# Kernel tuning notes

Hardware: AMD Instinct MI355X
Metric: run time of the kernel (lower is better)

Reference implementation:

```python
import jax, jax.numpy as jnp
import numpy as np

NOISE_EPS = 1e-2   # Shazeer noisy-gating stddev floor
LN_EPS = 1e-6
LOSS_COEF = 0.01
K = 2              # num_activated_experts


def _layer_norm(x, w, b):
    mu = jnp.mean(x, axis=-1, keepdims=True)
    var = jnp.var(x, axis=-1, keepdims=True)
    return (x - mu) * jax.lax.rsqrt(var + LN_EPS) * w + b


def _cv_squared(v):
    return jnp.var(v) / (jnp.mean(v) ** 2 + 1e-10)


def _normal_cdf(z):
    return 0.5 * (1.0 + jax.scipy.special.erf(z / jnp.sqrt(jnp.asarray(2.0, z.dtype))))


def setup_inputs() -> dict:
    key = jax.random.key(0)
    ks = jax.random.split(key, 8)
    N, D, H, O, E = 8192, 512, 1024, 512, 8
    x = jax.random.normal(ks[0], (N, D), jnp.float32)
    x_offsets = jnp.sort(jax.random.randint(ks[1], (17,), 0, N)).astype(jnp.int64)
    noise = jax.random.normal(ks[2], (N, E), jnp.float32)
    s = 0.02
    return {
        "x": x,
        "x_offsets": x_offsets,
        "max_seq_len": 2048,
        "noise": noise,
        "norm_w": jnp.ones((D,), jnp.float32),
        "norm_bias": jnp.zeros((D,), jnp.float32),
        "w_gate": jax.random.normal(ks[3], (D, E), jnp.float32) * s,
        "w_noise": jax.random.normal(ks[4], (D, E), jnp.float32) * s,
        "W1": jax.random.normal(ks[5], (E, H, D), jnp.float32) * s,  # [E, model_d, input]
        "b1": jnp.zeros((E, H), jnp.float32),
        "W2": jax.random.normal(ks[6], (E, O, H), jnp.float32) * s,  # [E, output, model_d]
        "b2": jnp.zeros((E, O), jnp.float32),
        "output_weight": jax.random.normal(ks[7], (D, O), jnp.float32) * s,
    }


def reference(x, x_offsets, max_seq_len, noise, norm_w, norm_bias, w_gate, w_noise,
              W1, b1, W2, b2, output_weight):
    N, D = x.shape
    E = w_gate.shape[1]
    k_plus = min(K + 1, E)

    # pre-norm
    x_norm = _layer_norm(x, norm_w, norm_bias)

    # noisy top-k gating (training path)
    clean_logits = x_norm @ w_gate                      # [N, E]
    noise_stddev = jax.nn.softplus(x_norm @ w_noise) + NOISE_EPS
    noisy_logits = clean_logits + noise * noise_stddev

    top_logits, top_indices = jax.lax.top_k(noisy_logits, k_plus)   # [N, k+1]
    top_k_logits = top_logits[:, :K]
    top_k_indices = top_indices[:, :K]
    top_k_gates = jax.nn.softmax(top_k_logits, axis=-1)             # [N, K]

    rows = jnp.arange(N)[:, None]
    gates = jnp.zeros((N, E), top_k_gates.dtype).at[rows, top_k_indices].set(top_k_gates)

    # load = prob each expert is in top-k under the gating noise (Shazeer)
    flat = top_logits.reshape(-1)
    pos_in = jnp.arange(N) * k_plus + K
    thr_in = flat[pos_in][:, None]          # (k+1)-th value: threshold if already in
    thr_out = flat[pos_in - 1][:, None]     # k-th value: threshold if currently out
    is_in = noisy_logits > thr_in
    prob_in = _normal_cdf((clean_logits - thr_in) / noise_stddev)
    prob_out = _normal_cdf((clean_logits - thr_out) / noise_stddev)
    load_probs = jnp.where(is_in, prob_in, prob_out)                # [N, E]

    loss = LOSS_COEF * (_cv_squared(gates.sum(0)) + _cv_squared(load_probs.sum(0)))

    # dispatch stats: tokens per expert
    lengths = jnp.zeros((E,), jnp.float32).at[top_k_indices.reshape(-1)].add(1.0)
    load = lengths / lengths.sum()

    # grouped expert MLP (dense one-hot combine; gates are 0 for unrouted experts)
    h = jnp.einsum('nd,ehd->neh', x_norm, W1) + b1                  # [N, E, H]
    a = jax.nn.silu(h)
    y_e = jnp.einsum('neh,eoh->neo', a, W2) + b2                    # [N, E, O]
    y_moe = jnp.einsum('ne,neo->no', gates, y_e)                    # [N, O]

    # shared expert: addmm(y, shared_x=x, output_weight)
    y = y_moe + x @ output_weight
    return y, loss, load
```

## Files before the change

### kernel.cpp

```cpp
#include <hip/hip_runtime.h>
#include <math.h>

typedef unsigned short u16;
typedef unsigned int u32;

#define N_ROWS 8192
#define DDIM 512
#define HDIM 1024
#define ODIM 512
#define NEXP 8
#define MAXPAIRS (N_ROWS * 2)
#define MAXPOS (MAXPAIRS + NEXP * 128)
#define MAXTILES (MAXPOS / 128)

#define SM_CNT 0
#define SM_CUR 8
#define SM_AOFF 16
#define SM_GSUM 32
#define SM_LSUM 40
#define SM_WORDS 64

using short8 = __attribute__((ext_vector_type(8))) short;
using float4v = __attribute__((ext_vector_type(4))) float;

__device__ __forceinline__ u16 f2bf(float f) {
    union { float f; u32 u; } v; v.f = f;
    u32 u = v.u;
    return (u16)((u + 0x7fffu + ((u >> 16) & 1u)) >> 16);
}

__device__ __forceinline__ void async_copy16(u16* lds, const u16* g) {
    __builtin_amdgcn_global_load_lds(
        (const __attribute__((address_space(1))) void*)g,
        (__attribute__((address_space(3))) void*)lds, 16, 0, 0);
}

#define CONV_BLOCKS 8192
__global__ __launch_bounds__(256) void prep_kernel(
    const float* __restrict__ W1, const float* __restrict__ W2, const float* __restrict__ ow,
    u16* __restrict__ W1b, u16* __restrict__ W2b, u16* __restrict__ owT,
    int* __restrict__ small, int* __restrict__ bucket_rows, float* __restrict__ zeropage)
{
    __shared__ float tile[32][33];
    int b = blockIdx.x, tid = threadIdx.x;
    if (b < CONV_BLOCKS) {
        const size_t n4 = (size_t)NEXP * HDIM * DDIM / 4;
        size_t i = (size_t)b * 256 + tid;
        const float* src; u16* dst;
        if (i < n4) { src = W1; dst = W1b; } else { src = W2; dst = W2b; i -= n4; }
        float4 v = ((const float4*)src)[i];
        ushort4 o;
        o.x = f2bf(v.x); o.y = f2bf(v.y); o.z = f2bf(v.z); o.w = f2bf(v.w);
        ((ushort4*)dst)[i] = o;
    } else if (b < CONV_BLOCKS + 256) {
        int t = b - CONV_BLOCKS;
        int bx = (t & 15) * 32, by = (t >> 4) * 32;
        int tx = tid & 31, ty = tid >> 5;
        for (int r = ty; r < 32; r += 8) tile[r][tx] = ow[(size_t)(by + r) * ODIM + bx + tx];
        __syncthreads();
        for (int r = ty; r < 32; r += 8) owT[(size_t)(bx + r) * DDIM + by + tx] = f2bf(tile[tx][r]);
    } else {
        int i = (b - CONV_BLOCKS - 256) * 256 + tid;
        if (i < SM_WORDS) small[i] = 0;
        if (i < 512) zeropage[i] = 0.f;
        if (i < MAXPOS) bucket_rows[i] = -1;
    }
}

__global__ __launch_bounds__(256) void gating_kernel(
    const float* __restrict__ x, const float* __restrict__ noise,
    const float* __restrict__ norm_w, const float* __restrict__ norm_b,
    const float* __restrict__ w_gate, const float* __restrict__ w_noise,
    u16* __restrict__ xnorm_bf, u16* __restrict__ x_bf,
    int* __restrict__ pair_expert, float* __restrict__ pair_gate,
    int* __restrict__ small)
{
    __shared__ float wgT[NEXP * DDIM];
    __shared__ float wnT[NEXP * DDIM];
    __shared__ float blk_g[NEXP];
    __shared__ float blk_l[NEXP];
    __shared__ int blk_c[NEXP];
    float* smf = (float*)small;

    int tid = threadIdx.x;
    for (int i = tid; i < NEXP * DDIM; i += 256) {
        int d = i >> 3, e = i & 7;
        wgT[e * DDIM + d] = w_gate[i];
        wnT[e * DDIM + d] = w_noise[i];
    }
    if (tid < NEXP) { blk_g[tid] = 0.f; blk_l[tid] = 0.f; blk_c[tid] = 0; }
    __syncthreads();

    int wave = tid >> 6, lane = tid & 63;
    float nw[8], nb[8];
#pragma unroll
    for (int j = 0; j < 8; j++) { nw[j] = norm_w[j * 64 + lane]; nb[j] = norm_b[j * 64 + lane]; }

    for (int r = 0; r < 4; ++r) {
        int row = blockIdx.x * 16 + wave * 4 + r;
        const float* xr = x + (size_t)row * DDIM;
        float xv[8], s = 0.f, s2 = 0.f;
#pragma unroll
        for (int j = 0; j < 8; j++) { float v = xr[j * 64 + lane]; xv[j] = v; s += v; s2 += v * v; }
#pragma unroll
        for (int o = 32; o; o >>= 1) { s += __shfl_xor(s, o, 64); s2 += __shfl_xor(s2, o, 64); }
        float mu = s * (1.f / DDIM);
        float var = s2 * (1.f / DDIM) - mu * mu;
        float rstd = rsqrtf(var + 1e-6f);

        float acc[16];
#pragma unroll
        for (int e = 0; e < 16; e++) acc[e] = 0.f;
#pragma unroll
        for (int j = 0; j < 8; j++) {
            float v = (xv[j] - mu) * rstd * nw[j] + nb[j];
            int d = j * 64 + lane;
            xnorm_bf[(size_t)row * DDIM + d] = f2bf(v);
            x_bf[(size_t)row * DDIM + d] = f2bf(xv[j]);
#pragma unroll
            for (int e = 0; e < 8; e++) {
                acc[e] += v * wgT[e * DDIM + d];
                acc[8 + e] += v * wnT[e * DDIM + d];
            }
        }
#pragma unroll
        for (int e = 0; e < 16; e++)
#pragma unroll
            for (int o = 32; o; o >>= 1) acc[e] += __shfl_xor(acc[e], o, 64);

        float cl[8], sd[8], nz[8];
#pragma unroll
        for (int e = 0; e < 8; e++) {
            cl[e] = acc[e];
            float t = acc[8 + e];
            float sp = fmaxf(t, 0.f) + log1pf(expf(-fabsf(t)));
            sd[e] = sp + 0.01f;
            nz[e] = cl[e] + noise[(size_t)row * NEXP + e] * sd[e];
        }
        int idx[3]; float val[3]; u32 msk = 0;
#pragma unroll
        for (int t = 0; t < 3; t++) {
            float best = -INFINITY; int bi = 0;
#pragma unroll
            for (int e = 0; e < 8; e++)
                if (!((msk >> e) & 1) && nz[e] > best) { best = nz[e]; bi = e; }
            idx[t] = bi; val[t] = best; msk |= 1u << bi;
        }
        float e1 = expf(val[1] - val[0]);
        float g0 = 1.f / (1.f + e1), g1 = e1 / (1.f + e1);
        float thr_in = val[2], thr_out = val[1];

        if (lane == 0) {
            pair_expert[row * 2] = idx[0]; pair_gate[row * 2] = g0;
            pair_expert[row * 2 + 1] = idx[1]; pair_gate[row * 2 + 1] = g1;
            atomicAdd(&blk_g[idx[0]], g0); atomicAdd(&blk_g[idx[1]], g1);
            atomicAdd(&blk_c[idx[0]], 1); atomicAdd(&blk_c[idx[1]], 1);
#pragma unroll
            for (int e = 0; e < 8; e++) {
                float thr = (nz[e] > thr_in) ? thr_in : thr_out;
                float z = (cl[e] - thr) / sd[e];
                float p = 0.5f * (1.f + erff(z * 0.70710678118654752f));
                atomicAdd(&blk_l[e], p);
            }
        }
    }
    __syncthreads();
    if (tid < NEXP) {
        atomicAdd(smf + SM_GSUM + tid, blk_g[tid]);
        atomicAdd(smf + SM_LSUM + tid, blk_l[tid]);
        atomicAdd(&small[SM_CNT + tid], blk_c[tid]);
    }
}

__global__ __launch_bounds__(256) void scatter_kernel(
    const int* __restrict__ pair_expert, const float* __restrict__ pair_gate,
    int* __restrict__ small, int* __restrict__ bucket_rows, float* __restrict__ gate_by_pos,
    float* __restrict__ out_loss, float* __restrict__ out_load)
{
    __shared__ int aoff[NEXP + 1];
    __shared__ int blk_cnt[NEXP];
    __shared__ int blk_base[NEXP];
    int tid = threadIdx.x;
    if (tid == 0) {
        int acc = 0; aoff[0] = 0;
        for (int e = 0; e < NEXP; e++) { acc += (small[SM_CNT + e] + 127) & ~127; aoff[e + 1] = acc; }
    }
    if (tid < NEXP) blk_cnt[tid] = 0;
    __syncthreads();
    int p = blockIdx.x * 256 + tid;
    int e = pair_expert[p];
    int local = atomicAdd(&blk_cnt[e], 1);
    __syncthreads();
    if (tid < NEXP)
        blk_base[tid] = aoff[tid] + atomicAdd(&small[SM_CUR + tid], blk_cnt[tid]);
    if (blockIdx.x == 0 && tid < NEXP + 1) small[SM_AOFF + tid] = aoff[tid];
    __syncthreads();
    int pos = blk_base[e] + local;
    bucket_rows[pos] = p >> 1;
    gate_by_pos[pos] = pair_gate[p];

    if (blockIdx.x == 0 && tid == 0) {
        const float* gs = (const float*)small + SM_GSUM;
        const float* ls = (const float*)small + SM_LSUM;
        float cv[2];
        for (int t = 0; t < 2; t++) {
            const float* v = t ? ls : gs;
            float m = 0.f;
            for (int k = 0; k < NEXP; k++) m += v[k];
            m *= (1.f / NEXP);
            float var = 0.f;
            for (int k = 0; k < NEXP; k++) { float d = v[k] - m; var += d * d; }
            var *= (1.f / NEXP);
            cv[t] = var / (m * m + 1e-10f);
        }
        out_loss[0] = 0.01f * (cv[0] + cv[1]);
        int tot = 0;
        for (int k = 0; k < NEXP; k++) tot += small[SM_CNT + k];
        float inv = 1.f / (float)tot;
        for (int k = 0; k < NEXP; k++) out_load[k] = (float)small[SM_CNT + k] * inv;
    }
}



__global__ __launch_bounds__(256) void gemmA_kernel(
    const u16* __restrict__ xnorm, const u16* __restrict__ xbf,
    const u16* __restrict__ W1b, const u16* __restrict__ owT,
    const int* __restrict__ bucket_rows, const int* __restrict__ small,
    const float* __restrict__ b1, const u16* __restrict__ zeropage,
    u16* __restrict__ a_buf, float* __restrict__ y)
{
    constexpr int KD = 512;
    __shared__ __align__(16) u16 As[128 * 64];
    __shared__ __align__(16) u16 Bs[128 * 64];

    int tid = threadIdx.x;
    bool m0 = blockIdx.y < 8;
    int base, bn, e = 0;
    const u16* Bsel;
    if (m0) {
        base = blockIdx.x * 128;
        if (base >= small[SM_AOFF + 8]) return;
        while (e < 7 && base >= small[SM_AOFF + e + 1]) ++e;
        bn = blockIdx.y * 128;
        Bsel = W1b + (size_t)e * HDIM * KD;
    } else {
        int j = (blockIdx.y - 8) * 136 + blockIdx.x;
        if (j >= 256) return;
        base = (j >> 2) * 128;
        bn = (j & 3) * 128;
        Bsel = owT;
    }

    int wave = tid >> 6, lane = tid & 63;
    int lr = lane >> 3;
    int lc = ((lane & 7) ^ lr) * 8;

    const u16* ga[4]; const u16* gb[4];
    u16* la[4]; u16* lb[4];
#pragma unroll
    for (int c = 0; c < 4; c++) {
        int tr = wave * 32 + c * 8;
        if (m0) {
            int r0 = bucket_rows[base + tr + lr];
            ga[c] = ((r0 < 0) ? zeropage : xnorm + (size_t)r0 * KD) + lc;
        } else {
            ga[c] = xbf + (size_t)(base + tr + lr) * KD + lc;
        }
        gb[c] = Bsel + (size_t)(bn + tr + lr) * KD + lc;
        la[c] = &As[tr * 64];
        lb[c] = &Bs[tr * 64];
    }

    int wm = (wave & 1) * 64, wn = (wave >> 1) * 64;
    int fr = lane & 15, kq = lane >> 4, f7 = fr & 7;

    float4v acc[4][4];
#pragma unroll
    for (int i = 0; i < 4; i++)
#pragma unroll
        for (int j = 0; j < 4; j++) acc[i][j] = (float4v){0.f, 0.f, 0.f, 0.f};

    for (int k0 = 0; k0 < KD; k0 += 64) {
        __syncthreads();
#pragma unroll
        for (int c = 0; c < 4; c++) async_copy16(la[c], ga[c] + k0);
#pragma unroll
        for (int c = 0; c < 4; c++) async_copy16(lb[c], gb[c] + k0);
        __syncthreads();
        short8 af[4][2], bf[4][2];
#pragma unroll
        for (int mt = 0; mt < 4; mt++)
#pragma unroll
            for (int kh = 0; kh < 2; kh++)
                af[mt][kh] = *(const short8*)&As[(wm + mt * 16 + fr) * 64 + (((kq + 4 * kh) ^ f7) * 8)];
#pragma unroll
        for (int nt = 0; nt < 4; nt++)
#pragma unroll
            for (int kh = 0; kh < 2; kh++)
                bf[nt][kh] = *(const short8*)&Bs[(wn + nt * 16 + fr) * 64 + (((kq + 4 * kh) ^ f7) * 8)];
#pragma unroll
        for (int mt = 0; mt < 4; mt++)
#pragma unroll
            for (int nt = 0; nt < 4; nt++) {
                acc[mt][nt] = __builtin_amdgcn_mfma_f32_16x16x32_bf16(af[mt][0], bf[nt][0], acc[mt][nt], 0, 0, 0);
                acc[mt][nt] = __builtin_amdgcn_mfma_f32_16x16x32_bf16(af[mt][1], bf[nt][1], acc[mt][nt], 0, 0, 0);
            }
    }

    int rbase = (lane >> 4) * 4, c16 = lane & 15;
#pragma unroll
    for (int nt = 0; nt < 4; nt++) {
        int gn = bn + wn + nt * 16 + c16;
        float bv = m0 ? b1[e * HDIM + gn] : 0.f;
#pragma unroll
        for (int mt = 0; mt < 4; mt++) {
            int gm = base + wm + mt * 16 + rbase;
#pragma unroll
            for (int r = 0; r < 4; r++) {
                float v = acc[mt][nt][r];
                if (m0) {
                    float h = v + bv;
                    float a = h * __builtin_amdgcn_rcpf(1.f + __expf(-h));
                    a_buf[(size_t)(gm + r) * HDIM + gn] = f2bf(a);
                } else {
                    y[(size_t)(gm + r) * ODIM + gn] = v;
                }
            }
        }
    }
}

__global__ __launch_bounds__(256) void gemmB_kernel(
    const u16* __restrict__ a_buf, const u16* __restrict__ W2b,
    const int* __restrict__ bucket_rows, const int* __restrict__ small,
    const float* __restrict__ b2, const float* __restrict__ gate_by_pos,
    float* __restrict__ y)
{
    constexpr int KD = 1024;
    __shared__ __align__(16) u16 As[128 * 64];
    __shared__ __align__(16) u16 Bs[64 * 64];

    int tid = threadIdx.x;
    int base = blockIdx.x * 128;
    if (base >= small[SM_AOFF + 8]) return;
    int e = 0;
    while (e < 7 && base >= small[SM_AOFF + e + 1]) ++e;
    int bn = blockIdx.y * 64;

    int wave = tid >> 6, lane = tid & 63;
    int lr = lane >> 3;
    int lc = ((lane & 7) ^ lr) * 8;

    const u16* Bsel = W2b + (size_t)e * ODIM * KD;
    const u16* ga[4]; const u16* gb[2];
    u16* la[4]; u16* lb[2];
#pragma unroll
    for (int c = 0; c < 4; c++) {
        int tr = wave * 32 + c * 8;
        ga[c] = a_buf + (size_t)(base + tr + lr) * KD + lc;
        la[c] = &As[tr * 64];
    }
#pragma unroll
    for (int c = 0; c < 2; c++) {
        int tr = wave * 16 + c * 8;
        gb[c] = Bsel + (size_t)(bn + tr + lr) * KD + lc;
        lb[c] = &Bs[tr * 64];
    }

    int wm = (wave & 1) * 64, wn = (wave >> 1) * 32;
    int fr = lane & 15, kq = lane >> 4, f7 = fr & 7;

    float4v acc[4][2];
#pragma unroll
    for (int i = 0; i < 4; i++)
#pragma unroll
        for (int j = 0; j < 2; j++) acc[i][j] = (float4v){0.f, 0.f, 0.f, 0.f};

    for (int k0 = 0; k0 < KD; k0 += 64) {
        __syncthreads();
#pragma unroll
        for (int c = 0; c < 4; c++) async_copy16(la[c], ga[c] + k0);
#pragma unroll
        for (int c = 0; c < 2; c++) async_copy16(lb[c], gb[c] + k0);
        __syncthreads();
        short8 af[4][2], bf[2][2];
#pragma unroll
        for (int mt = 0; mt < 4; mt++)
#pragma unroll
            for (int kh = 0; kh < 2; kh++)
                af[mt][kh] = *(const short8*)&As[(wm + mt * 16 + fr) * 64 + (((kq + 4 * kh) ^ f7) * 8)];
#pragma unroll
        for (int nt = 0; nt < 2; nt++)
#pragma unroll
            for (int kh = 0; kh < 2; kh++)
                bf[nt][kh] = *(const short8*)&Bs[(wn + nt * 16 + fr) * 64 + (((kq + 4 * kh) ^ f7) * 8)];
#pragma unroll
        for (int mt = 0; mt < 4; mt++)
#pragma unroll
            for (int nt = 0; nt < 2; nt++) {
                acc[mt][nt] = __builtin_amdgcn_mfma_f32_16x16x32_bf16(af[mt][0], bf[nt][0], acc[mt][nt], 0, 0, 0);
                acc[mt][nt] = __builtin_amdgcn_mfma_f32_16x16x32_bf16(af[mt][1], bf[nt][1], acc[mt][nt], 0, 0, 0);
            }
    }

    int rbase = (lane >> 4) * 4, c16 = lane & 15;
#pragma unroll
    for (int mt = 0; mt < 4; mt++) {
        int pos0 = base + wm + mt * 16 + rbase;
        int rows[4]; float gs[4];
#pragma unroll
        for (int r = 0; r < 4; r++) { rows[r] = bucket_rows[pos0 + r]; gs[r] = gate_by_pos[pos0 + r]; }
#pragma unroll
        for (int nt = 0; nt < 2; nt++) {
            int gn = bn + wn + nt * 16 + c16;
            float b2v = b2[e * ODIM + gn];
#pragma unroll
            for (int r = 0; r < 4; r++) {
                if (rows[r] >= 0)
                    unsafeAtomicAdd(&y[(size_t)rows[r] * ODIM + gn], gs[r] * (acc[mt][nt][r] + b2v));
            }
        }
    }
}

extern "C" void kernel_launch(void* const* d_in, const int* in_sizes, int n_in,
                              void* d_out, int out_size, void* d_ws, size_t ws_size,
                              hipStream_t stream)
{
    (void)in_sizes; (void)n_in; (void)out_size; (void)ws_size;
    const float* x = (const float*)d_in[0];
    const float* noise = (const float*)d_in[3];
    const float* norm_w = (const float*)d_in[4];
    const float* norm_b = (const float*)d_in[5];
    const float* w_gate = (const float*)d_in[6];
    const float* w_noise = (const float*)d_in[7];
    const float* W1 = (const float*)d_in[8];
    const float* b1 = (const float*)d_in[9];
    const float* W2 = (const float*)d_in[10];
    const float* b2 = (const float*)d_in[11];
    const float* ow = (const float*)d_in[12];

    float* y = (float*)d_out;
    float* out_loss = y + (size_t)N_ROWS * ODIM;
    float* out_load = out_loss + 1;

    char* ws = (char*)d_ws;
    size_t off = 0;
    auto alloc = [&](size_t b) { size_t p = off; off = (off + b + 255) & ~(size_t)255; return p; };
    u16* xnorm_bf = (u16*)(ws + alloc((size_t)N_ROWS * DDIM * 2));
    u16* x_bf     = (u16*)(ws + alloc((size_t)N_ROWS * DDIM * 2));
    u16* W1b      = (u16*)(ws + alloc((size_t)NEXP * HDIM * DDIM * 2));
    u16* W2b      = (u16*)(ws + alloc((size_t)NEXP * ODIM * HDIM * 2));
    u16* owT      = (u16*)(ws + alloc((size_t)DDIM * ODIM * 2));
    u16* a_buf    = (u16*)(ws + alloc((size_t)MAXPOS * HDIM * 2));
    int* pair_expert = (int*)(ws + alloc((size_t)MAXPAIRS * 4));
    float* pair_gate = (float*)(ws + alloc((size_t)MAXPAIRS * 4));
    float* gate_by_pos = (float*)(ws + alloc((size_t)MAXPOS * 4));
    int* bucket_rows = (int*)(ws + alloc((size_t)MAXPOS * 4));
    int* small       = (int*)(ws + alloc(SM_WORDS * 4));
    float* zeropage  = (float*)(ws + alloc(2048));

    prep_kernel<<<CONV_BLOCKS + 256 + 68, 256, 0, stream>>>(W1, W2, ow, W1b, W2b, owT,
                                                            small, bucket_rows, zeropage);
    gating_kernel<<<N_ROWS / 16, 256, 0, stream>>>(x, noise, norm_w, norm_b, w_gate, w_noise,
                                                   xnorm_bf, x_bf, pair_expert, pair_gate, small);
    scatter_kernel<<<MAXPAIRS / 256, 256, 0, stream>>>(pair_expert, pair_gate, small,
                                                       bucket_rows, gate_by_pos, out_loss, out_load);
    gemmA_kernel<<<dim3(MAXTILES, 10), 256, 0, stream>>>(xnorm_bf, x_bf, W1b, owT, bucket_rows,
                                                         small, b1, (const u16*)zeropage, a_buf, y);
    gemmB_kernel<<<dim3(MAXTILES, ODIM / 64), 256, 0, stream>>>(a_buf, W2b, bucket_rows, small,
                                                                b2, gate_by_pos, y);
}
```

Measured before the change: 271.0 us.

## Merge weight conversion into gating kernel and widen gemmB tile to 128x128

After: 279.5 us. 1.03x slower.

```diff
diff --git a/kernel.cpp b/kernel.cpp
--- a/kernel.cpp
+++ b/kernel.cpp
@@ -35,54 +35,60 @@
         (__attribute__((address_space(3))) void*)lds, 16, 0, 0);
 }
 
+__global__ __launch_bounds__(512) void init1_kernel(int* small, float* zeropage) {
+    int i = threadIdx.x;
+    if (i < SM_WORDS) small[i] = 0;
+    zeropage[i] = 0.f;
+}
+
 #define CONV_BLOCKS 8192
-__global__ __launch_bounds__(256) void prep_kernel(
-    const float* __restrict__ W1, const float* __restrict__ W2, const float* __restrict__ ow,
-    u16* __restrict__ W1b, u16* __restrict__ W2b, u16* __restrict__ owT,
-    int* __restrict__ small, int* __restrict__ bucket_rows, float* __restrict__ zeropage)
-{
-    __shared__ float tile[32][33];
-    int b = blockIdx.x, tid = threadIdx.x;
-    if (b < CONV_BLOCKS) {
-        const size_t n4 = (size_t)NEXP * HDIM * DDIM / 4;
-        size_t i = (size_t)b * 256 + tid;
-        const float* src; u16* dst;
-        if (i < n4) { src = W1; dst = W1b; } else { src = W2; dst = W2b; i -= n4; }
-        float4 v = ((const float4*)src)[i];
-        ushort4 o;
-        o.x = f2bf(v.x); o.y = f2bf(v.y); o.z = f2bf(v.z); o.w = f2bf(v.w);
-        ((ushort4*)dst)[i] = o;
-    } else if (b < CONV_BLOCKS + 256) {
-        int t = b - CONV_BLOCKS;
-        int bx = (t & 15) * 32, by = (t >> 4) * 32;
-        int tx = tid & 31, ty = tid >> 5;
-        for (int r = ty; r < 32; r += 8) tile[r][tx] = ow[(size_t)(by + r) * ODIM + bx + tx];
-        __syncthreads();
-        for (int r = ty; r < 32; r += 8) owT[(size_t)(bx + r) * DDIM + by + tx] = f2bf(tile[tx][r]);
-    } else {
-        int i = (b - CONV_BLOCKS - 256) * 256 + tid;
-        if (i < SM_WORDS) small[i] = 0;
-        if (i < 512) zeropage[i] = 0.f;
-        if (i < MAXPOS) bucket_rows[i] = -1;
-    }
-}
-
-__global__ __launch_bounds__(256) void gating_kernel(
+#define GATE_BLOCKS 512
+__global__ __launch_bounds__(256) void combo_kernel(
     const float* __restrict__ x, const float* __restrict__ noise,
     const float* __restrict__ norm_w, const float* __restrict__ norm_b,
     const float* __restrict__ w_gate, const float* __restrict__ w_noise,
+    const float* __restrict__ W1, const float* __restrict__ W2, const float* __restrict__ ow,
     u16* __restrict__ xnorm_bf, u16* __restrict__ x_bf,
     int* __restrict__ pair_expert, float* __restrict__ pair_gate,
-    int* __restrict__ small)
+    u16* __restrict__ W1b, u16* __restrict__ W2b, u16* __restrict__ owT,
+    int* __restrict__ small, int* __restrict__ bucket_rows)
 {
-    __shared__ float wgT[NEXP * DDIM];
-    __shared__ float wnT[NEXP * DDIM];
-    __shared__ float blk_g[NEXP];
-    __shared__ float blk_l[NEXP];
-    __shared__ int blk_c[NEXP];
+    __shared__ __align__(16) float sh[NEXP * DDIM * 2 + 64];
+    int b = blockIdx.x, tid = threadIdx.x;
+
+    if (b >= GATE_BLOCKS) {
+        int cb = b - GATE_BLOCKS;
+        if (cb < CONV_BLOCKS) {
+            const size_t n4 = (size_t)NEXP * HDIM * DDIM / 4;
+            size_t i = (size_t)cb * 256 + tid;
+            const float* src; u16* dst;
+            if (i < n4) { src = W1; dst = W1b; } else { src = W2; dst = W2b; i -= n4; }
+            float4 v = ((const float4*)src)[i];
+            ushort4 o;
+            o.x = f2bf(v.x); o.y = f2bf(v.y); o.z = f2bf(v.z); o.w = f2bf(v.w);
+            ((ushort4*)dst)[i] = o;
+        } else if (cb < CONV_BLOCKS + 256) {
+            float (*tile)[33] = (float(*)[33])sh;
+            int t = cb - CONV_BLOCKS;
+            int bx = (t & 15) * 32, by = (t >> 4) * 32;
+            int tx = tid & 31, ty = tid >> 5;
+            for (int r = ty; r < 32; r += 8) tile[r][tx] = ow[(size_t)(by + r) * ODIM + bx + tx];
+            __syncthreads();
+            for (int r = ty; r < 32; r += 8) owT[(size_t)(bx + r) * DDIM + by + tx] = f2bf(tile[tx][r]);
+        } else {
+            int i = (cb - CONV_BLOCKS - 256) * 256 + tid;
+            if (i < MAXPOS) bucket_rows[i] = -1;
+        }
+        return;
+    }
+
+    float* wgT = sh;
+    float* wnT = sh + NEXP * DDIM;
+    float* blk_g = sh + 2 * NEXP * DDIM;
+    float* blk_l = blk_g + NEXP;
+    int* blk_c = (int*)(blk_l + NEXP);
     float* smf = (float*)small;
 
-    int tid = threadIdx.x;
     for (int i = tid; i < NEXP * DDIM; i += 256) {
         int d = i >> 3, e = i & 7;
         wgT[e * DDIM + d] = w_gate[i];
@@ -97,7 +103,7 @@
     for (int j = 0; j < 8; j++) { nw[j] = norm_w[j * 64 + lane]; nb[j] = norm_b[j * 64 + lane]; }
 
     for (int r = 0; r < 4; ++r) {
-        int row = blockIdx.x * 16 + wave * 4 + r;
+        int row = b * 16 + wave * 4 + r;
         const float* xr = x + (size_t)row * DDIM;
         float xv[8], s = 0.f, s2 = 0.f;
 #pragma unroll
@@ -220,7 +226,6 @@
         for (int k = 0; k < NEXP; k++) out_load[k] = (float)small[SM_CNT + k] * inv;
     }
 }
-
 
 
 __global__ __launch_bounds__(256) void gemmA_kernel(
@@ -339,66 +344,62 @@
 {
     constexpr int KD = 1024;
     __shared__ __align__(16) u16 As[128 * 64];
-    __shared__ __align__(16) u16 Bs[64 * 64];
+    __shared__ __align__(16) u16 Bs[128 * 64];
 
     int tid = threadIdx.x;
     int base = blockIdx.x * 128;
     if (base >= small[SM_AOFF + 8]) return;
     int e = 0;
     while (e < 7 && base >= small[SM_AOFF + e + 1]) ++e;
-    int bn = blockIdx.y * 64;
+    int bn = blockIdx.y * 128;
 
     int wave = tid >> 6, lane = tid & 63;
     int lr = lane >> 3;
     int lc = ((lane & 7) ^ lr) * 8;
 
     const u16* Bsel = W2b + (size_t)e * ODIM * KD;
-    const u16* ga[4]; const u16* gb[2];
-    u16* la[4]; u16* lb[2];
+    const u16* ga[4]; const u16* gb[4];
+    u16* la[4]; u16* lb[4];
 #pragma unroll
     for (int c = 0; c < 4; c++) {
         int tr = wave * 32 + c * 8;
         ga[c] = a_buf + (size_t)(base + tr + lr) * KD + lc;
+        gb[c] = Bsel + (size_t)(bn + tr + lr) * KD + lc;
         la[c] = &As[tr * 64];
-    }
-#pragma unroll
-    for (int c = 0; c < 2; c++) {
-        int tr = wave * 16 + c * 8;
-        gb[c] = Bsel + (size_t)(bn + tr + lr) * KD + lc;
         lb[c] = &Bs[tr * 64];
     }
 
-    int wm = (wave & 1) * 64, wn = (wave >> 1) * 32;
+    int wm = (wave & 1) * 64, wn = (wave >> 1) * 64;
     int fr = lane & 15, kq = lane >> 4, f7 = fr & 7;
 
-    float4v acc[4][2];
+    float4v acc[4][4];
 #pragma unroll
     for (int i = 0; i < 4; i++)
 #pragma unroll
-        for (int j = 0; j < 2; j++) acc[i][j] = (float4v){0.f, 0.f, 0.f, 0.f};
+        for (int j = 0; j < 4; j++) acc[i][j] = (float4v){0.f, 0.f, 0.f, 0.f};
 
     for (int k0 = 0; k0 < KD; k0 += 64) {
         __syncthreads();
 #pragma unroll
         for (int c = 0; c < 4; c++) async_copy16(la[c], ga[c] + k0);
 #pragma unroll
-        for (int c = 0; c < 2; c++) async_copy16(lb[c], gb[c] + k0);
+        for (int c = 0; c < 4; c++) async_copy16(lb[c], gb[c] + k0);
         __syncthreads();
-        short8 af[4][2], bf[2][2];
+        short8 af[4][2], bf[4][2];
 #pragma unroll
         for (int mt = 0; mt < 4; mt++)
 #pragma unroll
             for (int kh = 0; kh < 2; kh++)
                 af[mt][kh] = *(const short8*)&As[(wm + mt * 16 + fr) * 64 + (((kq + 4 * kh) ^ f7) * 8)];
 #pragma unroll
-        for (int nt = 0; nt < 2; nt++)
+        for (int nt = 0; nt < 4; nt++)
 #pragma unroll
             for (int kh = 0; kh < 2; kh++)
                 bf[nt][kh] = *(const short8*)&Bs[(wn + nt * 16 + fr) * 64 + (((kq + 4 * kh) ^ f7) * 8)];
 #pragma unroll
         for (int mt = 0; mt < 4; mt++)
 #pragma unroll
-            for (int nt = 0; nt < 2; nt++) {
+            for (int nt = 0; nt < 4; nt++) {
                 acc[mt][nt] = __builtin_amdgcn_mfma_f32_16x16x32_bf16(af[mt][0], bf[nt][0], acc[mt][nt], 0, 0, 0);
                 acc[mt][nt] = __builtin_amdgcn_mfma_f32_16x16x32_bf16(af[mt][1], bf[nt][1], acc[mt][nt], 0, 0, 0);
             }
@@ -412,7 +413,7 @@
 #pragma unroll
         for (int r = 0; r < 4; r++) { rows[r] = bucket_rows[pos0 + r]; gs[r] = gate_by_pos[pos0 + r]; }
 #pragma unroll
-        for (int nt = 0; nt < 2; nt++) {
+        for (int nt = 0; nt < 4; nt++) {
             int gn = bn + wn + nt * 16 + c16;
             float b2v = b2[e * ODIM + gn];
 #pragma unroll
@@ -461,14 +462,14 @@
     int* small       = (int*)(ws + alloc(SM_WORDS * 4));
     float* zeropage  = (float*)(ws + alloc(2048));
 
-    prep_kernel<<<CONV_BLOCKS + 256 + 68, 256, 0, stream>>>(W1, W2, ow, W1b, W2b, owT,
-                                                            small, bucket_rows, zeropage);
-    gating_kernel<<<N_ROWS / 16, 256, 0, stream>>>(x, noise, norm_w, norm_b, w_gate, w_noise,
-                                                   xnorm_bf, x_bf, pair_expert, pair_gate, small);
+    init1_kernel<<<1, 512, 0, stream>>>(small, zeropage);
+    combo_kernel<<<GATE_BLOCKS + CONV_BLOCKS + 256 + 68, 256, 0, stream>>>(
+        x, noise, norm_w, norm_b, w_gate, w_noise, W1, W2, ow,
+        xnorm_bf, x_bf, pair_expert, pair_gate, W1b, W2b, owT, small, bucket_rows);
     scatter_kernel<<<MAXPAIRS / 256, 256, 0, stream>>>(pair_expert, pair_gate, small,
                                                        bucket_rows, gate_by_pos, out_loss, out_load);
     gemmA_kernel<<<dim3(MAXTILES, 10), 256, 0, stream>>>(xnorm_bf, x_bf, W1b, owT, bucket_rows,
                                                          small, b1, (const u16*)zeropage, a_buf, y);
-    gemmB_kernel<<<dim3(MAXTILES, ODIM / 64), 256, 0, stream>>>(a_buf, W2b, bucket_rows, small,
-                                                                b2, gate_by_pos, y);
-}
+    gemmB_kernel<<<dim3(MAXTILES, ODIM / 128), 256, 0, stream>>>(a_buf, W2b, bucket_rows, small,
+                                                                 b2, gate_by_pos, y);
+}
```
